# Kernel tuning notes

Measured on AMD Instinct MI355X. Metric: run time of the kernel, lower is better.

Reference implementation:

```python
import jax, jax.numpy as jnp
import numpy as np

B, S, E, H = 2, 2048, 1024, 16
D = E // H  # head dim = 64


def setup_inputs() -> dict:
    key = jax.random.key(0)
    ks = jax.random.split(key, 9)
    sc = 0.02
    return {
        "inputs": jax.random.normal(ks[0], (B, S, E), jnp.float32),
        "Wq": jax.random.normal(ks[1], (E, E), jnp.float32) * sc,
        "bq": jnp.zeros((E,), jnp.float32),
        "Wk": jax.random.normal(ks[2], (E, E), jnp.float32) * sc,
        "bk": jnp.zeros((E,), jnp.float32),
        "Wv": jax.random.normal(ks[3], (E, E), jnp.float32) * sc,
        "bv": jnp.zeros((E,), jnp.float32),
        "Wo": jax.random.normal(ks[4], (E, E), jnp.float32) * sc,
        "bo": jnp.zeros((E,), jnp.float32),
    }


def _split_heads(x):
    # [B, S, E] -> [B, H, S, D]
    b, s, _ = x.shape
    return x.reshape(b, s, H, D).transpose(0, 2, 1, 3)


def reference(inputs, Wq, bq, Wk, bk, Wv, bv, Wo, bo):
    q = _split_heads(inputs @ Wq + bq)
    k = _split_heads(inputs @ Wk + bk)
    v = _split_heads(inputs @ Wv + bv)

    # scaled dot-product scores: [B, H, S, S]
    score = jnp.einsum("bhqd,bhkd->bhqk", q, k) / jnp.sqrt(jnp.float32(D))

    # causal mask, exactly as the original: score*mask - 10000*(1-mask)
    i = jnp.arange(S)[:, None]
    j = jnp.arange(S)[None, :]
    mask = (i >= j).astype(score.dtype)  # square case of i >= j - S + S
    score = score * mask - 10000.0 * (1.0 - mask)

    weights = jax.nn.softmax(score, axis=-1)
    attn = jnp.einsum("bhqk,bhkd->bhqd", weights, v)  # [B, H, S, D]
    attn = attn.transpose(0, 2, 1, 3).reshape(inputs.shape[0], S, E)
    return attn @ Wo + bo
```

## Files before the change

### kernel.cpp

```cpp
#include <hip/hip_runtime.h>
#include <stdint.h>

#define Bc 2
#define Sc 2048
#define Ec 1024
#define Hc 16
#define Dc 64
#define Mc (Bc*Sc)

typedef __attribute__((ext_vector_type(4))) float f32x4;
typedef __attribute__((ext_vector_type(8))) short bf16x8v;
typedef __attribute__((ext_vector_type(4))) short bf16x4v;

#define SCL 0.1803368801f

__device__ __forceinline__ unsigned short f2bf(float f){
  unsigned int u = __float_as_uint(f);
  u += 0x7FFFu + ((u >> 16) & 1u);
  return (unsigned short)(u >> 16);
}

__device__ __forceinline__ unsigned int cvt_pk_bf16(float a, float b){
  unsigned int d;
  asm("v_cvt_pk_bf16_f32 %0, %1, %2" : "=v"(d) : "v"(a), "v"(b));
  return d;
}

__device__ __forceinline__ float fast_exp2(float x){
  float r;
  asm("v_exp_f32 %0, %1" : "=v"(r) : "v"(x));
  return r;
}

#define GLDS(src, dst) __builtin_amdgcn_global_load_lds( \
    (const __attribute__((address_space(1))) void*)(src), \
    (__attribute__((address_space(3))) void*)(dst), 16, 0, 0)

#define VMCNT(n) do { asm volatile("s_waitcnt vmcnt(" #n ")" ::: "memory"); \
                      __builtin_amdgcn_sched_barrier(0); } while(0)
#define BARRIER() do { __builtin_amdgcn_s_barrier(); \
                       __builtin_amdgcn_sched_barrier(0); } while(0)

__global__ __launch_bounds__(256) void k_prep(const float* __restrict__ X,
                                              unsigned short* __restrict__ Xb,
                                              const float* __restrict__ W0, const float* __restrict__ W1,
                                              const float* __restrict__ W2, const float* __restrict__ W3,
                                              unsigned short* __restrict__ WT4){
  __shared__ float st[64][65];
  int bx = blockIdx.x, t = threadIdx.x;
  if (bx < 4096){
    int i = bx*256 + t;
    float4 v = ((const float4*)X)[i];
    ushort4 o;
    o.x = f2bf(v.x); o.y = f2bf(v.y); o.z = f2bf(v.z); o.w = f2bf(v.w);
    ((ushort4*)Xb)[i] = o;
  } else {
    int id = bx - 4096;
    int z = id >> 8, rem = id & 255;
    int k0 = (rem >> 4)*64, n0 = (rem & 15)*64;
    const float* W = (z==0)?W0 : (z==1)?W1 : (z==2)?W2 : W3;
    unsigned short* o = WT4 + (size_t)z * Ec * Ec;
    #pragma unroll
    for (int i=0;i<16;i++){ int lin=i*256+t; int r=lin>>6, c=lin&63;
      st[r][c] = W[(size_t)(k0+r)*Ec + n0+c]; }
    __syncthreads();
    #pragma unroll
    for (int i=0;i<16;i++){ int lin=i*256+t; int nn=lin>>6, kk=lin&63;
      o[(size_t)(n0+nn)*Ec + k0+kk] = f2bf(st[kk][nn]); }
  }
}

__global__ __launch_bounds__(256,2) void k_qkv(const unsigned short* __restrict__ A,
                                               const unsigned short* __restrict__ WT4,
                                               const float* __restrict__ bq,
                                               const float* __restrict__ bk,
                                               const float* __restrict__ bv,
                                               unsigned short* __restrict__ QKV){
  __shared__ unsigned short sA[2][128*64];
  __shared__ unsigned short sB[2][3][64*64];
  int bm = blockIdx.y, bn = blockIdx.x;
  int t = threadIdx.x, w = t>>6, lane = t&63, quad = lane>>4, m16 = lane&15;
  int wm = w>>1, wn = w&1, sw = m16 & 7;
  f32x4 acc[3][4][2];
  #pragma unroll
  for (int z=0;z<3;z++)
    #pragma unroll
    for (int i=0;i<4;i++)
      #pragma unroll
      for (int j=0;j<2;j++) acc[z][i][j] = (f32x4){0.f,0.f,0.f,0.f};

  auto stage = [&](int kt, int buf){
    #pragma unroll
    for (int i=0;i<4;i++){
      int cb = (w*4 + i)*64;
      int L = cb + lane;
      int row = L>>3, c = (L&7) ^ (row&7);
      GLDS(A + (size_t)(bm*128 + row)*Ec + kt*64 + c*8, &sA[buf][0] + cb*8);
    }
    #pragma unroll
    for (int z=0;z<3;z++)
      #pragma unroll
      for (int i=0;i<2;i++){
        int cb = (w*2 + i)*64;
        int L = cb + lane;
        int row = L>>3, c = (L&7) ^ (row&7);
        GLDS(WT4 + (size_t)z*Ec*Ec + (size_t)(bn*64 + row)*Ec + kt*64 + c*8,
             &sB[buf][z][0] + cb*8);
      }
  };

  stage(0, 0);
  stage(1, 1);
  for (int kt=0; kt<Ec/64; ++kt){
    int cur = kt & 1;
    if (kt < Ec/64 - 1) VMCNT(10);
    else                VMCNT(0);
    BARRIER();
    bf16x8v af[4][2];
    #pragma unroll
    for (int s=0;s<4;s++){
      int row = wm*64 + s*16 + m16;
      af[s][0] = *(const bf16x8v*)(&sA[cur][0] + row*64 + ((quad  )^sw)*8);
      af[s][1] = *(const bf16x8v*)(&sA[cur][0] + row*64 + ((quad+4)^sw)*8);
    }
    #pragma unroll
    for (int z=0;z<3;z++){
      bf16x8v bfr[2][2];
      #pragma unroll
      for (int sn=0;sn<2;sn++){
        int rowb = wn*32 + sn*16 + m16;
        bfr[sn][0] = *(const bf16x8v*)(&sB[cur][z][0] + rowb*64 + ((quad  )^sw)*8);
        bfr[sn][1] = *(const bf16x8v*)(&sB[cur][z][0] + rowb*64 + ((quad+4)^sw)*8);
      }
      #pragma unroll
      for (int sm=0;sm<4;sm++)
        #pragma unroll
        for (int sn=0;sn<2;sn++){
          acc[z][sm][sn] = __builtin_amdgcn_mfma_f32_16x16x32_bf16(af[sm][0], bfr[sn][0], acc[z][sm][sn], 0,0,0);
          acc[z][sm][sn] = __builtin_amdgcn_mfma_f32_16x16x32_bf16(af[sm][1], bfr[sn][1], acc[z][sm][sn], 0,0,0);
        }
    }
    BARRIER();
    if (kt+2 < Ec/64) stage(kt+2, cur);
  }
  #pragma unroll
  for (int z=0;z<3;z++){
    const float* bias = (z==0)?bq : (z==1)?bk : bv;
    unsigned short* Out = QKV + (size_t)z * (size_t)Mc * Ec;
    #pragma unroll
    for (int sm=0;sm<4;sm++){
      int row0 = bm*128 + wm*64 + sm*16 + quad*4;
      int bidx = row0 >> 11;
      #pragma unroll
      for (int sn=0;sn<2;sn++){
        int col = bn*64 + wn*32 + sn*16 + m16;
        float bb = bias[col];
        int h = col >> 6, d = col & 63;
        if (z == 2){
          int s0 = (row0 & (Sc-1)) ^ ((d & 8) ? 4 : 0);
          ushort4 pk;
          pk.x = f2bf(acc[z][sm][sn][0] + bb);
          pk.y = f2bf(acc[z][sm][sn][1] + bb);
          pk.z = f2bf(acc[z][sm][sn][2] + bb);
          pk.w = f2bf(acc[z][sm][sn][3] + bb);
          *(ushort4*)(Out + (((size_t)bidx*Hc + h)*Dc + d)*Sc + s0) = pk;
        } else {
          float sc_ = (z==0) ? SCL : 1.0f;
          #pragma unroll
          for (int r=0;r<4;r++){
            int s = (row0 + r) & (Sc-1);
            Out[(((size_t)bidx*Hc + h)*Sc + s)*Dc + d] = f2bf((acc[z][sm][sn][r] + bb)*sc_);
          }
        }
      }
    }
  }
}

__global__ __launch_bounds__(256,3) void k_gemm1(const unsigned short* __restrict__ A,
                                                 const unsigned short* __restrict__ WT,
                                                 const float* __restrict__ bias,
                                                 float* __restrict__ Out){
  __shared__ unsigned short sA[2][128*64];
  __shared__ unsigned short sB[2][64*64];
  int bm = blockIdx.y, bn = blockIdx.x;
  int t = threadIdx.x, w = t>>6, lane = t&63, quad = lane>>4, m16 = lane&15;
  int wm = w>>1, wn = w&1, sw = m16 & 7;
  f32x4 acc[4][2];
  #pragma unroll
  for (int i=0;i<4;i++)
    #pragma unroll
    for (int j=0;j<2;j++) acc[i][j] = (f32x4){0.f,0.f,0.f,0.f};

  auto stage = [&](int kt, int buf){
    #pragma unroll
    for (int i=0;i<4;i++){
      int cb = (w*4 + i)*64;
      int L = cb + lane;
      int row = L>>3, c = (L&7) ^ (row&7);
      GLDS(A + (size_t)(bm*128 + row)*Ec + kt*64 + c*8, &sA[buf][0] + cb*8);
    }
    #pragma unroll
    for (int i=0;i<2;i++){
      int cb = (w*2 + i)*64;
      int L = cb + lane;
      int row = L>>3, c = (L&7) ^ (row&7);
      GLDS(WT + (size_t)(bn*64 + row)*Ec + kt*64 + c*8, &sB[buf][0] + cb*8);
    }
  };

  stage(0, 0);
  stage(1, 1);
  for (int kt=0; kt<Ec/64; ++kt){
    int cur = kt & 1;
    if (kt < Ec/64 - 1) VMCNT(6);
    else                VMCNT(0);
    BARRIER();
    bf16x8v af[4][2], bfr[2][2];
    #pragma unroll
    for (int s=0;s<4;s++){
      int row = wm*64 + s*16 + m16;
      af[s][0] = *(const bf16x8v*)(&sA[cur][0] + row*64 + ((quad  )^sw)*8);
      af[s][1] = *(const bf16x8v*)(&sA[cur][0] + row*64 + ((quad+4)^sw)*8);
    }
    #pragma unroll
    for (int sn=0;sn<2;sn++){
      int rowb = wn*32 + sn*16 + m16;
      bfr[sn][0] = *(const bf16x8v*)(&sB[cur][0] + rowb*64 + ((quad  )^sw)*8);
      bfr[sn][1] = *(const bf16x8v*)(&sB[cur][0] + rowb*64 + ((quad+4)^sw)*8);
    }
    #pragma unroll
    for (int sm=0;sm<4;sm++)
      #pragma unroll
      for (int sn=0;sn<2;sn++){
        acc[sm][sn] = __builtin_amdgcn_mfma_f32_16x16x32_bf16(af[sm][0], bfr[sn][0], acc[sm][sn], 0,0,0);
        acc[sm][sn] = __builtin_amdgcn_mfma_f32_16x16x32_bf16(af[sm][1], bfr[sn][1], acc[sm][sn], 0,0,0);
      }
    BARRIER();
    if (kt+2 < Ec/64) stage(kt+2, cur);
  }
  #pragma unroll
  for (int sm=0;sm<4;sm++){
    int row0 = bm*128 + wm*64 + sm*16 + quad*4;
    #pragma unroll
    for (int sn=0;sn<2;sn++){
      int col = bn*64 + wn*32 + sn*16 + m16;
      float bb = bias[col];
      #pragma unroll
      for (int r=0;r<4;r++)
        Out[(size_t)(row0+r)*Ec + col] = acc[sm][sn][r] + bb;
    }
  }
}

__device__ __forceinline__ void attn_tile(const unsigned short* sK, const unsigned short* sVT,
                                          bf16x8v qf0, bf16x8v qf1,
                                          bf16x4v ones4, f32x4& li, f32x4* Oa,
                                          int kbase, int qw, int quad, int m16){
  int sw = m16 & 7;
  f32x4 sc[4];
  #pragma unroll
  for (int sm=0;sm<4;sm++){
    int row = sm*16 + m16;
    bf16x8v kf0 = *(const bf16x8v*)(sK + row*64 + ((quad  )^sw)*8);
    bf16x8v kf1 = *(const bf16x8v*)(sK + row*64 + ((quad+4)^sw)*8);
    f32x4 a = (f32x4){0.f,0.f,0.f,0.f};
    a = __builtin_amdgcn_mfma_f32_16x16x32_bf16(kf0, qf0, a, 0,0,0);
    a = __builtin_amdgcn_mfma_f32_16x16x32_bf16(kf1, qf1, a, 0,0,0);
    sc[sm] = a;
  }
  if (kbase + 63 > qw){
    #pragma unroll
    for (int sm=0;sm<4;sm++)
      #pragma unroll
      for (int r=0;r<4;r++){
        int kg = kbase + sm*16 + quad*4 + r;
        float p = fast_exp2(sc[sm][r]);
        sc[sm][r] = (kg <= qw + m16) ? p : 0.0f;
      }
  } else {
    #pragma unroll
    for (int sm=0;sm<4;sm++)
      #pragma unroll
      for (int r=0;r<4;r++) sc[sm][r] = fast_exp2(sc[sm][r]);
  }

  bf16x4v a16[4];
  #pragma unroll
  for (int sm=0;sm<4;sm++){
    uint2 pk;
    pk.x = cvt_pk_bf16(sc[sm][0], sc[sm][1]);
    pk.y = cvt_pk_bf16(sc[sm][2], sc[sm][3]);
    a16[sm] = __builtin_bit_cast(bf16x4v, pk);
  }

  #pragma unroll
  for (int sm=0;sm<4;sm++)
    li = __builtin_amdgcn_mfma_f32_16x16x16bf16_1k(a16[sm], ones4, li, 0,0,0);

  int half = ((quad & 1) ^ (m16 >> 3)) * 4;
  #pragma unroll
  for (int tt=0;tt<4;tt++){
    int rowv = tt*16 + m16;
    #pragma unroll
    for (int sm=0;sm<4;sm++){
      uint2 vv = *(const uint2*)(sVT + rowv*64 + (((sm*2 + (quad>>1))^sw)*8) + half);
      Oa[tt] = __builtin_amdgcn_mfma_f32_16x16x16bf16_1k(a16[sm], __builtin_bit_cast(bf16x4v, vv), Oa[tt], 0,0,0);
    }
  }
}

__global__ __launch_bounds__(256,4) void k_attn(const unsigned short* __restrict__ Qb,
                                                const unsigned short* __restrict__ Kb,
                                                const unsigned short* __restrict__ VTb,
                                                unsigned short* __restrict__ Ob){
  __shared__ unsigned short sK [2][64*64];
  __shared__ unsigned short sVT[2][64*64];
  int bid = (int)blockIdx.x + 32*(int)blockIdx.y;
  int g = bid >> 3;
  int h3 = g >> 2;
  int qt = (h3 & 8) ? (h3 ^ 7) : h3;
  int bh = (bid & 7) + ((g & 3) << 3);
  size_t base = (size_t)bh * Sc * Dc;
  const unsigned short* Q  = Qb  + base;
  const unsigned short* K  = Kb  + base;
  const unsigned short* VT = VTb + base;
  int t = threadIdx.x, w = t>>6, lane = t&63, quad = lane>>4, m16 = lane&15;
  int qw = qt*64 + w*16;

  bf16x8v q0 = *(const bf16x8v*)(Q + (size_t)(qw + m16)*Dc + quad*8);
  bf16x8v q1 = *(const bf16x8v*)(Q + (size_t)(qw + m16)*Dc + 32 + quad*8);

  bf16x4v ones4;
  #pragma unroll
  for (int i=0;i<4;i++) ones4[i] = (short)0x3F80;

  f32x4 Oa[4];
  #pragma unroll
  for (int i=0;i<4;i++) Oa[i] = (f32x4){0.f,0.f,0.f,0.f};
  f32x4 li = (f32x4){0.f,0.f,0.f,0.f};

  auto stage = [&](int kt, int buf){
    int kbase = kt*64;
    #pragma unroll
    for (int i=0;i<2;i++){
      int cb = (w*2 + i)*64;
      int L = cb + lane;
      int row = L>>3, p = L&7, c = p ^ (row&7);
      GLDS(K  + (size_t)(kbase+row)*Dc + c*8,        &sK[buf][0]  + cb*8);
      GLDS(VT + (size_t)row*Sc + kbase + c*8,        &sVT[buf][0] + cb*8);
    }
  };

  stage(0, 0);
  for (int kt=0; kt<=qt; ++kt){
    int cur = kt & 1;
    __syncthreads();
    if (kt < qt) stage(kt+1, cur^1);
    attn_tile(&sK[cur][0], &sVT[cur][0], q0, q1, ones4, li, Oa, kt*64, qw, quad, m16);
  }

  int b = bh >> 4, h = bh & 15;
  float iv[4];
  #pragma unroll
  for (int r=0;r<4;r++) iv[r] = 1.0f/li[r];
  #pragma unroll
  for (int tt=0;tt<4;tt++)
    #pragma unroll
    for (int r=0;r<4;r++){
      int e = h*64 + tt*16 + m16;
      int s = qw + quad*4 + r;
      Ob[((size_t)b*Sc + s)*Ec + e] = f2bf(Oa[tt][r]*iv[r]);
    }
}

extern "C" void kernel_launch(void* const* d_in, const int* in_sizes, int n_in,
                              void* d_out, int out_size, void* d_ws, size_t ws_size,
                              hipStream_t stream){
  const float* X  = (const float*)d_in[0];
  const float* Wq = (const float*)d_in[1];
  const float* bq = (const float*)d_in[2];
  const float* Wk = (const float*)d_in[3];
  const float* bk = (const float*)d_in[4];
  const float* Wv = (const float*)d_in[5];
  const float* bv = (const float*)d_in[6];
  const float* Wo = (const float*)d_in[7];
  const float* bo = (const float*)d_in[8];

  uint8_t* ws = (uint8_t*)d_ws;
  unsigned short* Xb  = (unsigned short*)(ws);
  unsigned short* WT4 = (unsigned short*)(ws + (size_t)(8u<<20));
  unsigned short* QKV = (unsigned short*)(ws + (size_t)(16u<<20));
  unsigned short* ATT = (unsigned short*)(ws + (size_t)(40u<<20));

  k_prep<<<dim3(5120), 256, 0, stream>>>(X, Xb, Wq, Wk, Wv, Wo, WT4);
  k_qkv<<<dim3(16,32), 256, 0, stream>>>(Xb, WT4, bq, bk, bv, QKV);
  k_attn<<<dim3(32,32), 256, 0, stream>>>(QKV, QKV + (size_t)Mc*Ec, QKV + 2*(size_t)Mc*Ec, ATT);
  k_gemm1<<<dim3(16,32), 256, 0, stream>>>(ATT, WT4 + (size_t)3*Ec*Ec, bo, (float*)d_out);
}
```

Baseline: 168.6 us.

## Process two adjacent query tiles per attention block to reuse K/V tiles

Each attention workgroup now handles two consecutive 64-row query tiles (qtA=2p, qtB=2p+1) and shares every staged K and V^T tile in LDS between both, halving global K/V loads and LDS staging per query row. The grid shrinks from 1024 to 512 blocks, with a new causal load-balancing permutation over tile pairs. Per-thread register use doubles (two sets of accumulators and Q fragments), so launch bounds drop to 2 waves per SIMD, which reduces occupancy and latency hiding.

```diff
diff --git a/kernel.cpp b/kernel.cpp
--- a/kernel.cpp
+++ b/kernel.cpp
@@ -253,50 +253,72 @@
   }
 }
 
-__device__ __forceinline__ void attn_tile(const unsigned short* sK, const unsigned short* sVT,
-                                          bf16x8v qf0, bf16x8v qf1,
-                                          bf16x4v ones4, f32x4& li, f32x4* Oa,
-                                          int kbase, int qw, int quad, int m16){
+__device__ __forceinline__ void attn_dual(const unsigned short* sK, const unsigned short* sVT,
+                                          bf16x8v qA0, bf16x8v qA1, bf16x8v qB0, bf16x8v qB1,
+                                          bf16x4v ones4, f32x4& liA, f32x4& liB,
+                                          f32x4* OaA, f32x4* OaB,
+                                          int kbase, int qwA, int qwB, int quad, int m16, bool doA){
   int sw = m16 & 7;
-  f32x4 sc[4];
+  f32x4 scA[4], scB[4];
   #pragma unroll
   for (int sm=0;sm<4;sm++){
     int row = sm*16 + m16;
     bf16x8v kf0 = *(const bf16x8v*)(sK + row*64 + ((quad  )^sw)*8);
     bf16x8v kf1 = *(const bf16x8v*)(sK + row*64 + ((quad+4)^sw)*8);
-    f32x4 a = (f32x4){0.f,0.f,0.f,0.f};
-    a = __builtin_amdgcn_mfma_f32_16x16x32_bf16(kf0, qf0, a, 0,0,0);
-    a = __builtin_amdgcn_mfma_f32_16x16x32_bf16(kf1, qf1, a, 0,0,0);
-    sc[sm] = a;
-  }
-  if (kbase + 63 > qw){
-    #pragma unroll
-    for (int sm=0;sm<4;sm++)
+    f32x4 b = (f32x4){0.f,0.f,0.f,0.f};
+    b = __builtin_amdgcn_mfma_f32_16x16x32_bf16(kf0, qB0, b, 0,0,0);
+    b = __builtin_amdgcn_mfma_f32_16x16x32_bf16(kf1, qB1, b, 0,0,0);
+    scB[sm] = b;
+    if (doA){
+      f32x4 a = (f32x4){0.f,0.f,0.f,0.f};
+      a = __builtin_amdgcn_mfma_f32_16x16x32_bf16(kf0, qA0, a, 0,0,0);
+      a = __builtin_amdgcn_mfma_f32_16x16x32_bf16(kf1, qA1, a, 0,0,0);
+      scA[sm] = a;
+    }
+  }
+  bf16x4v a16A[4], a16B[4];
+  bool maskB = (kbase + 63 > qwB);
+  #pragma unroll
+  for (int sm=0;sm<4;sm++){
+    #pragma unroll
+    for (int r=0;r<4;r++){
+      float pv = fast_exp2(scB[sm][r]);
+      if (maskB){
+        int kg = kbase + sm*16 + quad*4 + r;
+        pv = (kg <= qwB + m16) ? pv : 0.0f;
+      }
+      scB[sm][r] = pv;
+    }
+    uint2 pk;
+    pk.x = cvt_pk_bf16(scB[sm][0], scB[sm][1]);
+    pk.y = cvt_pk_bf16(scB[sm][2], scB[sm][3]);
+    a16B[sm] = __builtin_bit_cast(bf16x4v, pk);
+  }
+  if (doA){
+    bool maskA = (kbase + 63 > qwA);
+    #pragma unroll
+    for (int sm=0;sm<4;sm++){
       #pragma unroll
       for (int r=0;r<4;r++){
-        int kg = kbase + sm*16 + quad*4 + r;
-        float p = fast_exp2(sc[sm][r]);
-        sc[sm][r] = (kg <= qw + m16) ? p : 0.0f;
-      }
-  } else {
-    #pragma unroll
-    for (int sm=0;sm<4;sm++)
-      #pragma unroll
-      for (int r=0;r<4;r++) sc[sm][r] = fast_exp2(sc[sm][r]);
-  }
-
-  bf16x4v a16[4];
+        float pv = fast_exp2(scA[sm][r]);
+        if (maskA){
+          int kg = kbase + sm*16 + quad*4 + r;
+          pv = (kg <= qwA + m16) ? pv : 0.0f;
+        }
+        scA[sm][r] = pv;
+      }
+      uint2 pk;
+      pk.x = cvt_pk_bf16(scA[sm][0], scA[sm][1]);
+      pk.y = cvt_pk_bf16(scA[sm][2], scA[sm][3]);
+      a16A[sm] = __builtin_bit_cast(bf16x4v, pk);
+    }
+  }
+
   #pragma unroll
   for (int sm=0;sm<4;sm++){
-    uint2 pk;
-    pk.x = cvt_pk_bf16(sc[sm][0], sc[sm][1]);
-    pk.y = cvt_pk_bf16(sc[sm][2], sc[sm][3]);
-    a16[sm] = __builtin_bit_cast(bf16x4v, pk);
-  }
-
-  #pragma unroll
-  for (int sm=0;sm<4;sm++)
-    li = __builtin_amdgcn_mfma_f32_16x16x16bf16_1k(a16[sm], ones4, li, 0,0,0);
+    liB = __builtin_amdgcn_mfma_f32_16x16x16bf16_1k(a16B[sm], ones4, liB, 0,0,0);
+    if (doA) liA = __builtin_amdgcn_mfma_f32_16x16x16bf16_1k(a16A[sm], ones4, liA, 0,0,0);
+  }
 
   int half = ((quad & 1) ^ (m16 >> 3)) * 4;
   #pragma unroll
@@ -305,40 +327,46 @@
     #pragma unroll
     for (int sm=0;sm<4;sm++){
       uint2 vv = *(const uint2*)(sVT + rowv*64 + (((sm*2 + (quad>>1))^sw)*8) + half);
-      Oa[tt] = __builtin_amdgcn_mfma_f32_16x16x16bf16_1k(a16[sm], __builtin_bit_cast(bf16x4v, vv), Oa[tt], 0,0,0);
-    }
-  }
-}
-
-__global__ __launch_bounds__(256,4) void k_attn(const unsigned short* __restrict__ Qb,
+      bf16x4v vf = __builtin_bit_cast(bf16x4v, vv);
+      OaB[tt] = __builtin_amdgcn_mfma_f32_16x16x16bf16_1k(a16B[sm], vf, OaB[tt], 0,0,0);
+      if (doA) OaA[tt] = __builtin_amdgcn_mfma_f32_16x16x16bf16_1k(a16A[sm], vf, OaA[tt], 0,0,0);
+    }
+  }
+}
+
+__global__ __launch_bounds__(256,2) void k_attn(const unsigned short* __restrict__ Qb,
                                                 const unsigned short* __restrict__ Kb,
                                                 const unsigned short* __restrict__ VTb,
                                                 unsigned short* __restrict__ Ob){
   __shared__ unsigned short sK [2][64*64];
   __shared__ unsigned short sVT[2][64*64];
-  int bid = (int)blockIdx.x + 32*(int)blockIdx.y;
+  int bid = (int)blockIdx.x;
   int g = bid >> 3;
-  int h3 = g >> 2;
-  int qt = (h3 & 8) ? (h3 ^ 7) : h3;
-  int bh = (bid & 7) + ((g & 3) << 3);
+  int bh = (bid & 7) | ((g & 3) << 3);
+  int j  = g >> 2;
+  int p  = (j & 8) ? (15 - (j & 7)) : j;
+  int qtA = 2*p, qtB = 2*p + 1;
   size_t base = (size_t)bh * Sc * Dc;
   const unsigned short* Q  = Qb  + base;
   const unsigned short* K  = Kb  + base;
   const unsigned short* VT = VTb + base;
   int t = threadIdx.x, w = t>>6, lane = t&63, quad = lane>>4, m16 = lane&15;
-  int qw = qt*64 + w*16;
-
-  bf16x8v q0 = *(const bf16x8v*)(Q + (size_t)(qw + m16)*Dc + quad*8);
-  bf16x8v q1 = *(const bf16x8v*)(Q + (size_t)(qw + m16)*Dc + 32 + quad*8);
+  int qwA = qtA*64 + w*16;
+  int qwB = qtB*64 + w*16;
+
+  bf16x8v qA0 = *(const bf16x8v*)(Q + (size_t)(qwA + m16)*Dc + quad*8);
+  bf16x8v qA1 = *(const bf16x8v*)(Q + (size_t)(qwA + m16)*Dc + 32 + quad*8);
+  bf16x8v qB0 = *(const bf16x8v*)(Q + (size_t)(qwB + m16)*Dc + quad*8);
+  bf16x8v qB1 = *(const bf16x8v*)(Q + (size_t)(qwB + m16)*Dc + 32 + quad*8);
 
   bf16x4v ones4;
   #pragma unroll
   for (int i=0;i<4;i++) ones4[i] = (short)0x3F80;
 
-  f32x4 Oa[4];
-  #pragma unroll
-  for (int i=0;i<4;i++) Oa[i] = (f32x4){0.f,0.f,0.f,0.f};
-  f32x4 li = (f32x4){0.f,0.f,0.f,0.f};
+  f32x4 OaA[4], OaB[4];
+  #pragma unroll
+  for (int i=0;i<4;i++){ OaA[i] = (f32x4){0.f,0.f,0.f,0.f}; OaB[i] = (f32x4){0.f,0.f,0.f,0.f}; }
+  f32x4 liA = (f32x4){0.f,0.f,0.f,0.f}, liB = (f32x4){0.f,0.f,0.f,0.f};
 
   auto stage = [&](int kt, int buf){
     int kbase = kt*64;
@@ -346,31 +374,34 @@
     for (int i=0;i<2;i++){
       int cb = (w*2 + i)*64;
       int L = cb + lane;
-      int row = L>>3, p = L&7, c = p ^ (row&7);
+      int row = L>>3, pp = L&7, c = pp ^ (row&7);
       GLDS(K  + (size_t)(kbase+row)*Dc + c*8,        &sK[buf][0]  + cb*8);
       GLDS(VT + (size_t)row*Sc + kbase + c*8,        &sVT[buf][0] + cb*8);
     }
   };
 
   stage(0, 0);
-  for (int kt=0; kt<=qt; ++kt){
+  for (int kt=0; kt<=qtB; ++kt){
     int cur = kt & 1;
     __syncthreads();
-    if (kt < qt) stage(kt+1, cur^1);
-    attn_tile(&sK[cur][0], &sVT[cur][0], q0, q1, ones4, li, Oa, kt*64, qw, quad, m16);
+    if (kt < qtB) stage(kt+1, cur^1);
+    attn_dual(&sK[cur][0], &sVT[cur][0], qA0, qA1, qB0, qB1, ones4,
+              liA, liB, OaA, OaB, kt*64, qwA, qwB, quad, m16, kt <= qtA);
   }
 
   int b = bh >> 4, h = bh & 15;
-  float iv[4];
-  #pragma unroll
-  for (int r=0;r<4;r++) iv[r] = 1.0f/li[r];
+  float iA[4], iB[4];
+  #pragma unroll
+  for (int r=0;r<4;r++){ iA[r] = 1.0f/liA[r]; iB[r] = 1.0f/liB[r]; }
   #pragma unroll
   for (int tt=0;tt<4;tt++)
     #pragma unroll
     for (int r=0;r<4;r++){
       int e = h*64 + tt*16 + m16;
-      int s = qw + quad*4 + r;
-      Ob[((size_t)b*Sc + s)*Ec + e] = f2bf(Oa[tt][r]*iv[r]);
+      int sA_ = qwA + quad*4 + r;
+      int sB_ = qwB + quad*4 + r;
+      Ob[((size_t)b*Sc + sA_)*Ec + e] = f2bf(OaA[tt][r]*iA[r]);
+      Ob[((size_t)b*Sc + sB_)*Ec + e] = f2bf(OaB[tt][r]*iB[r]);
     }
 }
 
@@ -395,6 +426,6 @@
 
   k_prep<<<dim3(5120), 256, 0, stream>>>(X, Xb, Wq, Wk, Wv, Wo, WT4);
   k_qkv<<<dim3(16,32), 256, 0, stream>>>(Xb, WT4, bq, bk, bv, QKV);
-  k_attn<<<dim3(32,32), 256, 0, stream>>>(QKV, QKV + (size_t)Mc*Ec, QKV + 2*(size_t)Mc*Ec, ATT);
+  k_attn<<<dim3(512), 256, 0, stream>>>(QKV, QKV + (size_t)Mc*Ec, QKV + 2*(size_t)Mc*Ec, ATT);
   k_gemm1<<<dim3(16,32), 256, 0, stream>>>(ATT, WT4 + (size_t)3*Ec*Ec, bo, (float*)d_out);
 }
```

Result: slower. 203.0 us (+20.4%).
